# Performance work log

Hardware: AMD Instinct MI355X
Metric: run time of the kernel (lower is better)

The kernel has to match this reference:

```python
import jax, jax.numpy as jnp
import numpy as np

N, B, E = 10000, 4, 160000
C_IN, C_OUT, C_E = 64, 64, 16


def _mk_params(key, c_in, c_out, c_e):
    ks = jax.random.split(key, 8)
    s = 0.1
    return dict(
        w_n=jax.random.normal(ks[0], (c_in, c_out), jnp.float32) * s,
        w_e=jax.random.normal(ks[1], (c_e, c_out), jnp.float32) * s,
        q=jax.random.normal(ks[2], (c_out, c_out), jnp.float32) * s,
        k=jax.random.normal(ks[3], (c_out, c_out), jnp.float32) * s,
        aw=jax.random.normal(ks[4], (3 * c_out, 1), jnp.float32) * s,
        ab=jax.random.normal(ks[5], (1,), jnp.float32) * s,
        ow=jax.random.normal(ks[6], (2 * c_out, c_out), jnp.float32) * s,
        ob=jax.random.normal(ks[7], (c_out,), jnp.float32) * s,
    )


def setup_inputs() -> dict:
    key = jax.random.key(0)
    kx, ke, ka, k1, k2 = jax.random.split(key, 5)
    inp = {
        'X': jax.random.normal(kx, (N, B, C_IN), jnp.float32),
        'edge_index': jax.random.randint(ke, (2, E), 0, N, jnp.int32),
        'edge_attr': jax.random.normal(ka, (E, C_E), jnp.float32),
    }
    p1 = _mk_params(k1, C_IN, C_OUT, C_E)
    p2 = _mk_params(k2, C_OUT, C_OUT, C_E)
    for name, v in p1.items():
        inp[name + '1'] = v
    for name, v in p2.items():
        inp[name + '2'] = v
    return inp


def egnn_conv(x, edge_index, edge_attr, w_n, w_e, q, k, aw, ab, ow, ob, n_nodes):
    # x: [N,B,Cin]; edge_attr: [E,Ce]
    xp = x @ w_n                         # [N,B,C]
    ea = edge_attr @ w_e                 # [E,C]
    src, dst = edge_index[0], edge_index[1]
    xj = xp[src]                         # [E,B,C] gather (source)
    xi = xp[dst]                         # [E,B,C] gather (target)
    qf = xj @ q                          # [E,B,C]
    kf = xi @ k                          # [E,B,C]
    eab = jnp.broadcast_to(ea[:, None, :], qf.shape)  # [E,B,C]
    att_feat = jnp.concatenate([qf, kf, eab], axis=-1)  # [E,B,3C]
    att = jax.nn.sigmoid(att_feat @ aw + ab)            # [E,B,1]
    gate = jax.nn.sigmoid(eab)
    msg = att * xj * gate                # [E,B,C]
    aggr = jax.ops.segment_max(msg, dst, num_segments=n_nodes)  # [N,B,C]
    aggr = jnp.where(jnp.isneginf(aggr), 0.0, aggr)  # empty segments -> 0
    out = jnp.concatenate([xp, aggr], axis=-1) @ ow + ob
    return xp + out


def reference(X, edge_index, edge_attr,
              w_n1, w_e1, q1, k1, aw1, ab1, ow1, ob1,
              w_n2, w_e2, q2, k2, aw2, ab2, ow2, ob2):
    n_nodes = X.shape[0]
    c1 = egnn_conv(X, edge_index, edge_attr, w_n1, w_e1, q1, k1, aw1, ab1, ow1, ob1, n_nodes)
    c1 = jax.nn.leaky_relu(c1, 0.01)
    c2 = egnn_conv(c1, edge_index, edge_attr, w_n2, w_e2, q2, k2, aw2, ab2, ow2, ob2, n_nodes)
    c2 = jax.nn.leaky_relu(c2, 0.01)
    return c2
```

## Files before the change

kernel.cpp:

```cpp
#include <hip/hip_runtime.h>
#include <math.h>

#define NN 10000
#define BB 4
#define EE 160000
#define CC 64
#define CE 16

static constexpr size_t OFF_XPA    = 0;
static constexpr size_t OFF_XPB    = 10240000;
static constexpr size_t OFF_AGG    = 20480000;
static constexpr size_t OFF_SA     = 30720000;
static constexpr size_t OFF_SB     = 30880000;
static constexpr size_t OFF_VECS   = 31040000;
static constexpr size_t OFF_COUNTS = 31041280;
static constexpr size_t OFF_CURSOR = 31081280;
static constexpr size_t OFF_OFFS   = 31121280;
static constexpr size_t OFF_RECS   = 31161344;
static constexpr size_t OFF_ATT    = 32441344;

__device__ __forceinline__ float sigmoidf_(float x) {
    return 1.0f / (1.0f + __expf(-x));
}

__global__ void hist_vecs_kernel(const int* __restrict__ ei, int* __restrict__ counts,
                                 const float* __restrict__ q1, const float* __restrict__ k1,
                                 const float* __restrict__ aw1, const float* __restrict__ we1,
                                 const float* __restrict__ q2, const float* __restrict__ k2,
                                 const float* __restrict__ aw2, const float* __restrict__ we2,
                                 float* __restrict__ vecs) {
    int e = blockIdx.x * blockDim.x + threadIdx.x;
    if (e < EE) atomicAdd(&counts[ei[EE + e]], 1);
    if (blockIdx.x == 0) {
        int t = threadIdx.x;
        if (t < 64) {
            float a = 0.f, b = 0.f, c = 0.f, d = 0.f;
            for (int j = 0; j < 64; ++j) {
                a = fmaf(q1[t * 64 + j], aw1[j], a);
                b = fmaf(k1[t * 64 + j], aw1[64 + j], b);
                c = fmaf(q2[t * 64 + j], aw2[j], c);
                d = fmaf(k2[t * 64 + j], aw2[64 + j], d);
            }
            vecs[t] = a; vecs[64 + t] = b; vecs[144 + t] = c; vecs[208 + t] = d;
        }
        if (t < 16) {
            float a = 0.f, b = 0.f;
            for (int j = 0; j < 64; ++j) {
                a = fmaf(we1[t * 64 + j], aw1[128 + j], a);
                b = fmaf(we2[t * 64 + j], aw2[128 + j], b);
            }
            vecs[128 + t] = a; vecs[272 + t] = b;
        }
    }
}

__global__ void scan_kernel(const int* __restrict__ counts, int* __restrict__ offs, int n) {
    __shared__ int wsum[16];
    __shared__ int carry_sh;
    int t = threadIdx.x;
    int lane = t & 63, wid = t >> 6;
    if (t == 0) carry_sh = 0;
    __syncthreads();
    for (int base = 0; base < n; base += 1024) {
        int i = base + t;
        int v = (i < n) ? counts[i] : 0;
        int x = v;
        #pragma unroll
        for (int d = 1; d < 64; d <<= 1) {
            int y = __shfl_up(x, d, 64);
            if (lane >= d) x += y;
        }
        if (lane == 63) wsum[wid] = x;
        __syncthreads();
        if (wid == 0 && lane < 16) {
            int s = wsum[lane];
            int y2 = s;
            #pragma unroll
            for (int d = 1; d < 16; d <<= 1) {
                int z = __shfl_up(y2, d, 16);
                if (lane >= d) y2 += z;
            }
            wsum[lane] = y2;
        }
        __syncthreads();
        int waveExcl = (wid == 0) ? 0 : wsum[wid - 1];
        int carry = carry_sh;
        if (i < n) offs[i] = carry + waveExcl + x - v;
        int total = wsum[15];
        __syncthreads();
        if (t == 0) carry_sh = carry + total;
        __syncthreads();
    }
    if (threadIdx.x == 0) offs[n] = carry_sh;
}

__global__ void scatter_kernel(const int* __restrict__ ei, const int* __restrict__ offs,
                               int* __restrict__ cursor, int2* __restrict__ recs) {
    int e = blockIdx.x * blockDim.x + threadIdx.x;
    if (e >= EE) return;
    int s = ei[e], d = ei[EE + e];
    int p = atomicAdd(&cursor[d], 1);
    recs[offs[d] + p] = make_int2(s, e);
}

template <bool IN_T>
__global__ __launch_bounds__(256) void node_prep_kernel(
    const float* __restrict__ x,
    const float* __restrict__ w_n,
    const float* __restrict__ qa,
    const float* __restrict__ ka,
    float* __restrict__ xp_t,
    float* __restrict__ sa,
    float* __restrict__ sb) {
    __shared__ float w_sh[64 * 64];
    __shared__ float x_sh[4 * BB * CC];
    int t = threadIdx.x;
    for (int i = t; i < 64 * 64; i += 256) w_sh[i] = w_n[i];
    int node0 = blockIdx.x * 4;
    const float4* xg = (const float4*)(x + (size_t)node0 * BB * CC);
    ((float4*)x_sh)[t] = xg[t];
    __syncthreads();
    int wave = t >> 6, lane = t & 63;
    int node = node0 + wave;
    const float* xrow = x_sh + wave * BB * CC;
    float acc0 = 0.f, acc1 = 0.f, acc2 = 0.f, acc3 = 0.f;
    #pragma unroll 8
    for (int ci = 0; ci < 64; ++ci) {
        float w = w_sh[ci * 64 + lane];
        float x0 = IN_T ? xrow[ci * 4 + 0] : xrow[ci];
        float x1 = IN_T ? xrow[ci * 4 + 1] : xrow[64 + ci];
        float x2 = IN_T ? xrow[ci * 4 + 2] : xrow[128 + ci];
        float x3 = IN_T ? xrow[ci * 4 + 3] : xrow[192 + ci];
        acc0 = fmaf(x0, w, acc0);
        acc1 = fmaf(x1, w, acc1);
        acc2 = fmaf(x2, w, acc2);
        acc3 = fmaf(x3, w, acc3);
    }
    float4 st; st.x = acc0; st.y = acc1; st.z = acc2; st.w = acc3;
    *(float4*)(xp_t + (size_t)node * 256 + lane * 4) = st;
    float qv = qa[lane], kv = ka[lane];
    float ra0 = acc0 * qv, ra1 = acc1 * qv, ra2 = acc2 * qv, ra3 = acc3 * qv;
    float rb0 = acc0 * kv, rb1 = acc1 * kv, rb2 = acc2 * kv, rb3 = acc3 * kv;
    #pragma unroll
    for (int off = 32; off >= 1; off >>= 1) {
        ra0 += __shfl_xor(ra0, off, 64); ra1 += __shfl_xor(ra1, off, 64);
        ra2 += __shfl_xor(ra2, off, 64); ra3 += __shfl_xor(ra3, off, 64);
        rb0 += __shfl_xor(rb0, off, 64); rb1 += __shfl_xor(rb1, off, 64);
        rb2 += __shfl_xor(rb2, off, 64); rb3 += __shfl_xor(rb3, off, 64);
    }
    if (lane == 0) {
        sa[node * BB + 0] = ra0; sa[node * BB + 1] = ra1;
        sa[node * BB + 2] = ra2; sa[node * BB + 3] = ra3;
        sb[node * BB + 0] = rb0; sb[node * BB + 1] = rb1;
        sb[node * BB + 2] = rb2; sb[node * BB + 3] = rb3;
    }
}

__global__ __launch_bounds__(256) void att_kernel(
    const int* __restrict__ ei, const float* __restrict__ attr,
    const float* __restrict__ sa, const float* __restrict__ sb,
    const float* __restrict__ weav,
    const float* __restrict__ ab,
    float4* __restrict__ att) {
    int e = blockIdx.x * blockDim.x + threadIdx.x;
    if (e >= EE) return;
    int s = ei[e], d = ei[EE + e];
    const float4* ap = (const float4*)(attr + (size_t)e * CE);
    float4 a0 = ap[0], a1 = ap[1], a2 = ap[2], a3 = ap[3];
    float se = ab[0];
    se = fmaf(a0.x, weav[0], se);  se = fmaf(a0.y, weav[1], se);
    se = fmaf(a0.z, weav[2], se);  se = fmaf(a0.w, weav[3], se);
    se = fmaf(a1.x, weav[4], se);  se = fmaf(a1.y, weav[5], se);
    se = fmaf(a1.z, weav[6], se);  se = fmaf(a1.w, weav[7], se);
    se = fmaf(a2.x, weav[8], se);  se = fmaf(a2.y, weav[9], se);
    se = fmaf(a2.z, weav[10], se); se = fmaf(a2.w, weav[11], se);
    se = fmaf(a3.x, weav[12], se); se = fmaf(a3.y, weav[13], se);
    se = fmaf(a3.z, weav[14], se); se = fmaf(a3.w, weav[15], se);
    float4 sas = *(const float4*)(sa + (size_t)s * BB);
    float4 sbn = *(const float4*)(sb + (size_t)d * BB);
    float4 r;
    r.x = sigmoidf_(sas.x + sbn.x + se);
    r.y = sigmoidf_(sas.y + sbn.y + se);
    r.z = sigmoidf_(sas.z + sbn.z + se);
    r.w = sigmoidf_(sas.w + sbn.w + se);
    att[e] = r;
}

__global__ __launch_bounds__(256) void aggr_kernel(
    const float* __restrict__ xp_t,
    const int2* __restrict__ recs,
    const int* __restrict__ offs,
    const float* __restrict__ attr,
    const float* __restrict__ w_e,
    const float4* __restrict__ att,
    float* __restrict__ aggr_t) {
    int t = threadIdx.x;
    int wave = t >> 6, lane = t & 63;
    int node = blockIdx.x * 4 + wave;

    float wec[CE];
    #pragma unroll
    for (int j = 0; j < CE; ++j) wec[j] = w_e[j * CC + lane];

    int o0 = offs[node], o1 = offs[node + 1];
    float m0 = -INFINITY, m1 = -INFINITY, m2 = -INFINITY, m3 = -INFINITY;

    int i = o0;
    int2 rec = (i < o1) ? recs[i] : make_int2(0, 0);
    while (i < o1) {
        int2 cur = rec;
        ++i;
        if (i < o1) rec = recs[i];
        int s = cur.x, e = cur.y;
        float4 at = att[e];
        float4 xv = *(const float4*)(xp_t + (size_t)s * 256 + lane * 4);
        const float4* ap = (const float4*)(attr + (size_t)e * CE);
        float4 a0 = ap[0], a1 = ap[1], a2 = ap[2], a3 = ap[3];
        float g = 0.f;
        g = fmaf(a0.x, wec[0], g);  g = fmaf(a0.y, wec[1], g);
        g = fmaf(a0.z, wec[2], g);  g = fmaf(a0.w, wec[3], g);
        g = fmaf(a1.x, wec[4], g);  g = fmaf(a1.y, wec[5], g);
        g = fmaf(a1.z, wec[6], g);  g = fmaf(a1.w, wec[7], g);
        g = fmaf(a2.x, wec[8], g);  g = fmaf(a2.y, wec[9], g);
        g = fmaf(a2.z, wec[10], g); g = fmaf(a2.w, wec[11], g);
        g = fmaf(a3.x, wec[12], g); g = fmaf(a3.y, wec[13], g);
        g = fmaf(a3.z, wec[14], g); g = fmaf(a3.w, wec[15], g);
        g = sigmoidf_(g);
        m0 = fmaxf(m0, at.x * xv.x * g);
        m1 = fmaxf(m1, at.y * xv.y * g);
        m2 = fmaxf(m2, at.z * xv.z * g);
        m3 = fmaxf(m3, at.w * xv.w * g);
    }
    m0 = (m0 == -INFINITY) ? 0.f : m0;
    m1 = (m1 == -INFINITY) ? 0.f : m1;
    m2 = (m2 == -INFINITY) ? 0.f : m2;
    m3 = (m3 == -INFINITY) ? 0.f : m3;
    float4 st; st.x = m0; st.y = m1; st.z = m2; st.w = m3;
    *(float4*)(aggr_t + (size_t)node * 256 + lane * 4) = st;
}

template <bool WRITE_T>
__global__ __launch_bounds__(256) void out_kernel(
    const float* __restrict__ xp_t,
    const float* __restrict__ aggr_t,
    const float* __restrict__ ow,
    const float* __restrict__ ob,
    float* __restrict__ out) {
    __shared__ float xs[4][BB * CC];
    __shared__ float as_[4][BB * CC];
    int t = threadIdx.x;
    int wave = t >> 6, lane = t & 63;
    int node = blockIdx.x * 4 + wave;

    float4 xv = *(const float4*)(xp_t + (size_t)node * 256 + lane * 4);
    float4 av = *(const float4*)(aggr_t + (size_t)node * 256 + lane * 4);
    xs[wave][0 * 64 + lane] = xv.x; xs[wave][1 * 64 + lane] = xv.y;
    xs[wave][2 * 64 + lane] = xv.z; xs[wave][3 * 64 + lane] = xv.w;
    as_[wave][0 * 64 + lane] = av.x; as_[wave][1 * 64 + lane] = av.y;
    as_[wave][2 * 64 + lane] = av.z; as_[wave][3 * 64 + lane] = av.w;
    __syncthreads();

    const float* xr = xs[wave];
    const float* ar = as_[wave];
    float o0f = 0.f, o1f = 0.f, o2f = 0.f, o3f = 0.f;
    #pragma unroll 4
    for (int ci = 0; ci < 64; ++ci) {
        float wa = ow[ci * 64 + lane];
        float wb = ow[(64 + ci) * 64 + lane];
        o0f = fmaf(xr[ci], wa, o0f);
        o1f = fmaf(xr[64 + ci], wa, o1f);
        o2f = fmaf(xr[128 + ci], wa, o2f);
        o3f = fmaf(xr[192 + ci], wa, o3f);
        o0f = fmaf(ar[ci], wb, o0f);
        o1f = fmaf(ar[64 + ci], wb, o1f);
        o2f = fmaf(ar[128 + ci], wb, o2f);
        o3f = fmaf(ar[192 + ci], wb, o3f);
    }
    float obv = ob[lane];
    float r0 = xv.x + o0f + obv;
    float r1 = xv.y + o1f + obv;
    float r2 = xv.z + o2f + obv;
    float r3 = xv.w + o3f + obv;
    r0 = (r0 > 0.f) ? r0 : 0.01f * r0;
    r1 = (r1 > 0.f) ? r1 : 0.01f * r1;
    r2 = (r2 > 0.f) ? r2 : 0.01f * r2;
    r3 = (r3 > 0.f) ? r3 : 0.01f * r3;
    if (WRITE_T) {
        float4 st; st.x = r0; st.y = r1; st.z = r2; st.w = r3;
        *(float4*)(out + (size_t)node * 256 + lane * 4) = st;
    } else {
        float* op = out + (size_t)node * 256 + lane;
        op[0] = r0; op[64] = r1; op[128] = r2; op[192] = r3;
    }
}

extern "C" void kernel_launch(void* const* d_in, const int* in_sizes, int n_in,
                              void* d_out, int out_size, void* d_ws, size_t ws_size,
                              hipStream_t stream) {
    const float* X    = (const float*)d_in[0];
    const int*   ei   = (const int*)d_in[1];
    const float* attr = (const float*)d_in[2];
    const float* w_n1 = (const float*)d_in[3];
    const float* w_e1 = (const float*)d_in[4];
    const float* q1   = (const float*)d_in[5];
    const float* k1   = (const float*)d_in[6];
    const float* aw1  = (const float*)d_in[7];
    const float* ab1  = (const float*)d_in[8];
    const float* ow1  = (const float*)d_in[9];
    const float* ob1  = (const float*)d_in[10];
    const float* w_n2 = (const float*)d_in[11];
    const float* w_e2 = (const float*)d_in[12];
    const float* q2   = (const float*)d_in[13];
    const float* k2   = (const float*)d_in[14];
    const float* aw2  = (const float*)d_in[15];
    const float* ab2  = (const float*)d_in[16];
    const float* ow2  = (const float*)d_in[17];
    const float* ob2  = (const float*)d_in[18];
    float* out = (float*)d_out;

    char* ws = (char*)d_ws;
    float*  xpA    = (float*)(ws + OFF_XPA);
    float*  xpB    = (float*)(ws + OFF_XPB);
    float*  agg    = (float*)(ws + OFF_AGG);
    float*  sa     = (float*)(ws + OFF_SA);
    float*  sb     = (float*)(ws + OFF_SB);
    float*  vecs   = (float*)(ws + OFF_VECS);
    int*    counts = (int*)(ws + OFF_COUNTS);
    int*    cursor = (int*)(ws + OFF_CURSOR);
    int*    offs   = (int*)(ws + OFF_OFFS);
    int2*   recs   = (int2*)(ws + OFF_RECS);
    float4* att    = (float4*)(ws + OFF_ATT);

    hipMemsetAsync(counts, 0, 2 * NN * sizeof(int), stream);
    hist_vecs_kernel<<<EE / 256, 256, 0, stream>>>(ei, counts, q1, k1, aw1, w_e1,
                                                   q2, k2, aw2, w_e2, vecs);
    scan_kernel<<<1, 1024, 0, stream>>>(counts, offs, NN);
    scatter_kernel<<<EE / 256, 256, 0, stream>>>(ei, offs, cursor, recs);

    node_prep_kernel<false><<<NN / 4, 256, 0, stream>>>(X, w_n1, vecs + 0, vecs + 64,
                                                        xpA, sa, sb);
    att_kernel<<<EE / 256, 256, 0, stream>>>(ei, attr, sa, sb, vecs + 128, ab1, att);
    aggr_kernel<<<NN / 4, 256, 0, stream>>>(xpA, recs, offs, attr, w_e1, att, agg);
    out_kernel<true><<<NN / 4, 256, 0, stream>>>(xpA, agg, ow1, ob1, xpB);

    node_prep_kernel<true><<<NN / 4, 256, 0, stream>>>(xpB, w_n2, vecs + 144, vecs + 208,
                                                       xpA, sa, sb);
    att_kernel<<<EE / 256, 256, 0, stream>>>(ei, attr, sa, sb, vecs + 272, ab2, att);
    aggr_kernel<<<NN / 4, 256, 0, stream>>>(xpA, recs, offs, attr, w_e2, att, agg);
    out_kernel<false><<<NN / 4, 256, 0, stream>>>(xpA, agg, ow2, ob2, out);
}
```

Before: 316.8 us.

## Precompute per-edge gate tensor in edge kernel and unroll aggregation gather loop

The edge-attention kernel now also computes the sigmoid gate (edge_attr @ w_e) for all 64 channels per edge and writes it to a new E x 64 workspace buffer, one wave per 16 edges. The aggregation kernel then reads the precomputed gate instead of reloading edge attributes and redoing the 16-term dot product per edge, and processes four incoming edges per iteration to issue more independent gathers. The trade-off is about 41 MB of extra gate writes and reads per layer in exchange for less per-edge ALU work and fewer dependent loads in the aggregation loop.

```diff
diff --git a/kernel.cpp b/kernel.cpp
--- a/kernel.cpp
+++ b/kernel.cpp
@@ -18,6 +18,7 @@
 static constexpr size_t OFF_OFFS   = 31121280;
 static constexpr size_t OFF_RECS   = 31161344;
 static constexpr size_t OFF_ATT    = 32441344;
+static constexpr size_t OFF_GATE   = 35001344;
 
 __device__ __forceinline__ float sigmoidf_(float x) {
     return 1.0f / (1.0f + __expf(-x));
@@ -156,80 +157,99 @@
     }
 }
 
-__global__ __launch_bounds__(256) void att_kernel(
+__global__ __launch_bounds__(256) void edge_pre_kernel(
     const int* __restrict__ ei, const float* __restrict__ attr,
     const float* __restrict__ sa, const float* __restrict__ sb,
+    const float* __restrict__ w_e,
     const float* __restrict__ weav,
     const float* __restrict__ ab,
-    float4* __restrict__ att) {
-    int e = blockIdx.x * blockDim.x + threadIdx.x;
-    if (e >= EE) return;
-    int s = ei[e], d = ei[EE + e];
-    const float4* ap = (const float4*)(attr + (size_t)e * CE);
-    float4 a0 = ap[0], a1 = ap[1], a2 = ap[2], a3 = ap[3];
-    float se = ab[0];
-    se = fmaf(a0.x, weav[0], se);  se = fmaf(a0.y, weav[1], se);
-    se = fmaf(a0.z, weav[2], se);  se = fmaf(a0.w, weav[3], se);
-    se = fmaf(a1.x, weav[4], se);  se = fmaf(a1.y, weav[5], se);
-    se = fmaf(a1.z, weav[6], se);  se = fmaf(a1.w, weav[7], se);
-    se = fmaf(a2.x, weav[8], se);  se = fmaf(a2.y, weav[9], se);
-    se = fmaf(a2.z, weav[10], se); se = fmaf(a2.w, weav[11], se);
-    se = fmaf(a3.x, weav[12], se); se = fmaf(a3.y, weav[13], se);
-    se = fmaf(a3.z, weav[14], se); se = fmaf(a3.w, weav[15], se);
-    float4 sas = *(const float4*)(sa + (size_t)s * BB);
-    float4 sbn = *(const float4*)(sb + (size_t)d * BB);
-    float4 r;
-    r.x = sigmoidf_(sas.x + sbn.x + se);
-    r.y = sigmoidf_(sas.y + sbn.y + se);
-    r.z = sigmoidf_(sas.z + sbn.z + se);
-    r.w = sigmoidf_(sas.w + sbn.w + se);
-    att[e] = r;
+    float4* __restrict__ att, float* __restrict__ gate) {
+    int t = threadIdx.x;
+    int wave = t >> 6, lane = t & 63;
+    float wec[CE], wav[CE];
+    #pragma unroll
+    for (int j = 0; j < CE; ++j) { wec[j] = w_e[j * CC + lane]; wav[j] = weav[j]; }
+    float abv = ab[0];
+    int e0 = (blockIdx.x * 4 + wave) * 16;
+    #pragma unroll 2
+    for (int k = 0; k < 16; ++k) {
+        int e = e0 + k;
+        int s = ei[e], d = ei[EE + e];
+        const float4* ap = (const float4*)(attr + (size_t)e * CE);
+        float4 a0 = ap[0], a1 = ap[1], a2 = ap[2], a3 = ap[3];
+        float g = 0.f, se = 0.f;
+        g = fmaf(a0.x, wec[0], g);  se = fmaf(a0.x, wav[0], se);
+        g = fmaf(a0.y, wec[1], g);  se = fmaf(a0.y, wav[1], se);
+        g = fmaf(a0.z, wec[2], g);  se = fmaf(a0.z, wav[2], se);
+        g = fmaf(a0.w, wec[3], g);  se = fmaf(a0.w, wav[3], se);
+        g = fmaf(a1.x, wec[4], g);  se = fmaf(a1.x, wav[4], se);
+        g = fmaf(a1.y, wec[5], g);  se = fmaf(a1.y, wav[5], se);
+        g = fmaf(a1.z, wec[6], g);  se = fmaf(a1.z, wav[6], se);
+        g = fmaf(a1.w, wec[7], g);  se = fmaf(a1.w, wav[7], se);
+        g = fmaf(a2.x, wec[8], g);  se = fmaf(a2.x, wav[8], se);
+        g = fmaf(a2.y, wec[9], g);  se = fmaf(a2.y, wav[9], se);
+        g = fmaf(a2.z, wec[10], g); se = fmaf(a2.z, wav[10], se);
+        g = fmaf(a2.w, wec[11], g); se = fmaf(a2.w, wav[11], se);
+        g = fmaf(a3.x, wec[12], g); se = fmaf(a3.x, wav[12], se);
+        g = fmaf(a3.y, wec[13], g); se = fmaf(a3.y, wav[13], se);
+        g = fmaf(a3.z, wec[14], g); se = fmaf(a3.z, wav[14], se);
+        g = fmaf(a3.w, wec[15], g); se = fmaf(a3.w, wav[15], se);
+        gate[(size_t)e * CC + lane] = sigmoidf_(g);
+        float4 sas = *(const float4*)(sa + (size_t)s * BB);
+        float4 sbn = *(const float4*)(sb + (size_t)d * BB);
+        if (lane == 0) {
+            float4 r;
+            r.x = sigmoidf_(sas.x + sbn.x + se + abv);
+            r.y = sigmoidf_(sas.y + sbn.y + se + abv);
+            r.z = sigmoidf_(sas.z + sbn.z + se + abv);
+            r.w = sigmoidf_(sas.w + sbn.w + se + abv);
+            att[e] = r;
+        }
+    }
 }
 
 __global__ __launch_bounds__(256) void aggr_kernel(
     const float* __restrict__ xp_t,
     const int2* __restrict__ recs,
     const int* __restrict__ offs,
-    const float* __restrict__ attr,
-    const float* __restrict__ w_e,
     const float4* __restrict__ att,
+    const float* __restrict__ gate,
     float* __restrict__ aggr_t) {
     int t = threadIdx.x;
     int wave = t >> 6, lane = t & 63;
     int node = blockIdx.x * 4 + wave;
 
-    float wec[CE];
-    #pragma unroll
-    for (int j = 0; j < CE; ++j) wec[j] = w_e[j * CC + lane];
-
     int o0 = offs[node], o1 = offs[node + 1];
     float m0 = -INFINITY, m1 = -INFINITY, m2 = -INFINITY, m3 = -INFINITY;
 
     int i = o0;
-    int2 rec = (i < o1) ? recs[i] : make_int2(0, 0);
-    while (i < o1) {
-        int2 cur = rec;
-        ++i;
-        if (i < o1) rec = recs[i];
-        int s = cur.x, e = cur.y;
-        float4 at = att[e];
-        float4 xv = *(const float4*)(xp_t + (size_t)s * 256 + lane * 4);
-        const float4* ap = (const float4*)(attr + (size_t)e * CE);
-        float4 a0 = ap[0], a1 = ap[1], a2 = ap[2], a3 = ap[3];
-        float g = 0.f;
-        g = fmaf(a0.x, wec[0], g);  g = fmaf(a0.y, wec[1], g);
-        g = fmaf(a0.z, wec[2], g);  g = fmaf(a0.w, wec[3], g);
-        g = fmaf(a1.x, wec[4], g);  g = fmaf(a1.y, wec[5], g);
-        g = fmaf(a1.z, wec[6], g);  g = fmaf(a1.w, wec[7], g);
-        g = fmaf(a2.x, wec[8], g);  g = fmaf(a2.y, wec[9], g);
-        g = fmaf(a2.z, wec[10], g); g = fmaf(a2.w, wec[11], g);
-        g = fmaf(a3.x, wec[12], g); g = fmaf(a3.y, wec[13], g);
-        g = fmaf(a3.z, wec[14], g); g = fmaf(a3.w, wec[15], g);
-        g = sigmoidf_(g);
-        m0 = fmaxf(m0, at.x * xv.x * g);
-        m1 = fmaxf(m1, at.y * xv.y * g);
-        m2 = fmaxf(m2, at.z * xv.z * g);
-        m3 = fmaxf(m3, at.w * xv.w * g);
+    for (; i + 4 <= o1; i += 4) {
+        int2 ra = recs[i], rb = recs[i + 1], rc = recs[i + 2], rd = recs[i + 3];
+        float4 xa = *(const float4*)(xp_t + (size_t)ra.x * 256 + lane * 4);
+        float4 xb = *(const float4*)(xp_t + (size_t)rb.x * 256 + lane * 4);
+        float4 xc = *(const float4*)(xp_t + (size_t)rc.x * 256 + lane * 4);
+        float4 xd = *(const float4*)(xp_t + (size_t)rd.x * 256 + lane * 4);
+        float ga = gate[(size_t)ra.y * CC + lane];
+        float gb = gate[(size_t)rb.y * CC + lane];
+        float gc = gate[(size_t)rc.y * CC + lane];
+        float gd = gate[(size_t)rd.y * CC + lane];
+        float4 Aa = att[ra.y], Ab = att[rb.y], Ac = att[rc.y], Ad = att[rd.y];
+        m0 = fmaxf(m0, Aa.x * xa.x * ga); m1 = fmaxf(m1, Aa.y * xa.y * ga);
+        m2 = fmaxf(m2, Aa.z * xa.z * ga); m3 = fmaxf(m3, Aa.w * xa.w * ga);
+        m0 = fmaxf(m0, Ab.x * xb.x * gb); m1 = fmaxf(m1, Ab.y * xb.y * gb);
+        m2 = fmaxf(m2, Ab.z * xb.z * gb); m3 = fmaxf(m3, Ab.w * xb.w * gb);
+        m0 = fmaxf(m0, Ac.x * xc.x * gc); m1 = fmaxf(m1, Ac.y * xc.y * gc);
+        m2 = fmaxf(m2, Ac.z * xc.z * gc); m3 = fmaxf(m3, Ac.w * xc.w * gc);
+        m0 = fmaxf(m0, Ad.x * xd.x * gd); m1 = fmaxf(m1, Ad.y * xd.y * gd);
+        m2 = fmaxf(m2, Ad.z * xd.z * gd); m3 = fmaxf(m3, Ad.w * xd.w * gd);
+    }
+    for (; i < o1; ++i) {
+        int2 r = recs[i];
+        float4 xv = *(const float4*)(xp_t + (size_t)r.x * 256 + lane * 4);
+        float g = gate[(size_t)r.y * CC + lane];
+        float4 at = att[r.y];
+        m0 = fmaxf(m0, at.x * xv.x * g); m1 = fmaxf(m1, at.y * xv.y * g);
+        m2 = fmaxf(m2, at.z * xv.z * g); m3 = fmaxf(m3, at.w * xv.w * g);
     }
     m0 = (m0 == -INFINITY) ? 0.f : m0;
     m1 = (m1 == -INFINITY) ? 0.f : m1;
@@ -330,6 +350,7 @@
     int*    offs   = (int*)(ws + OFF_OFFS);
     int2*   recs   = (int2*)(ws + OFF_RECS);
     float4* att    = (float4*)(ws + OFF_ATT);
+    float*  gate   = (float*)(ws + OFF_GATE);
 
     hipMemsetAsync(counts, 0, 2 * NN * sizeof(int), stream);
     hist_vecs_kernel<<<EE / 256, 256, 0, stream>>>(ei, counts, q1, k1, aw1, w_e1,
@@ -339,13 +360,15 @@
 
     node_prep_kernel<false><<<NN / 4, 256, 0, stream>>>(X, w_n1, vecs + 0, vecs + 64,
                                                         xpA, sa, sb);
-    att_kernel<<<EE / 256, 256, 0, stream>>>(ei, attr, sa, sb, vecs + 128, ab1, att);
-    aggr_kernel<<<NN / 4, 256, 0, stream>>>(xpA, recs, offs, attr, w_e1, att, agg);
+    edge_pre_kernel<<<EE / 64, 256, 0, stream>>>(ei, attr, sa, sb, w_e1, vecs + 128,
+                                                 ab1, att, gate);
+    aggr_kernel<<<NN / 4, 256, 0, stream>>>(xpA, recs, offs, att, gate, agg);
     out_kernel<true><<<NN / 4, 256, 0, stream>>>(xpA, agg, ow1, ob1, xpB);
 
     node_prep_kernel<true><<<NN / 4, 256, 0, stream>>>(xpB, w_n2, vecs + 144, vecs + 208,
                                                        xpA, sa, sb);
-    att_kernel<<<EE / 256, 256, 0, stream>>>(ei, attr, sa, sb, vecs + 272, ab2, att);
-    aggr_kernel<<<NN / 4, 256, 0, stream>>>(xpA, recs, offs, attr, w_e2, att, agg);
+    edge_pre_kernel<<<EE / 64, 256, 0, stream>>>(ei, attr, sa, sb, w_e2, vecs + 272,
+                                                 ab2, att, gate);
+    aggr_kernel<<<NN / 4, 256, 0, stream>>>(xpA, recs, offs, att, gate, agg);
     out_kernel<false><<<NN / 4, 256, 0, stream>>>(xpA, agg, ow2, ob2, out);
 }
```

Result: slower. 371.8 us (+17.4%).

## Precompute per-edge gates in edge kernel and split node aggregation across four waves

Applied to the files above, without the earlier changes.

The per-edge sigmoid gate (edge_attr @ w_e) moves out of the aggregation loop into a per-edge kernel that also computes attention, writing a [E,64] gate buffer. Aggregation then runs one block per node, with four waves splitting the node's edge list and an LDS max-reduction combining them. This removes the repeated 16-FMA gate computation per gathered edge and adds parallelism for high-degree nodes. In exchange it writes and reads an extra 41 MB gate buffer per layer, and launches one wave per edge in the edge kernel.

```diff
diff --git a/kernel.cpp b/kernel.cpp
--- a/kernel.cpp
+++ b/kernel.cpp
@@ -18,6 +18,7 @@
 static constexpr size_t OFF_OFFS   = 31121280;
 static constexpr size_t OFF_RECS   = 31161344;
 static constexpr size_t OFF_ATT    = 32441344;
+static constexpr size_t OFF_GATE   = 35001344;
 
 __device__ __forceinline__ float sigmoidf_(float x) {
     return 1.0f / (1.0f + __expf(-x));
@@ -156,87 +157,107 @@
     }
 }
 
-__global__ __launch_bounds__(256) void att_kernel(
+__global__ __launch_bounds__(256) void edge_gate_att_kernel(
     const int* __restrict__ ei, const float* __restrict__ attr,
     const float* __restrict__ sa, const float* __restrict__ sb,
+    const float* __restrict__ w_e,
     const float* __restrict__ weav,
     const float* __restrict__ ab,
-    float4* __restrict__ att) {
-    int e = blockIdx.x * blockDim.x + threadIdx.x;
-    if (e >= EE) return;
-    int s = ei[e], d = ei[EE + e];
-    const float4* ap = (const float4*)(attr + (size_t)e * CE);
-    float4 a0 = ap[0], a1 = ap[1], a2 = ap[2], a3 = ap[3];
-    float se = ab[0];
-    se = fmaf(a0.x, weav[0], se);  se = fmaf(a0.y, weav[1], se);
-    se = fmaf(a0.z, weav[2], se);  se = fmaf(a0.w, weav[3], se);
-    se = fmaf(a1.x, weav[4], se);  se = fmaf(a1.y, weav[5], se);
-    se = fmaf(a1.z, weav[6], se);  se = fmaf(a1.w, weav[7], se);
-    se = fmaf(a2.x, weav[8], se);  se = fmaf(a2.y, weav[9], se);
-    se = fmaf(a2.z, weav[10], se); se = fmaf(a2.w, weav[11], se);
-    se = fmaf(a3.x, weav[12], se); se = fmaf(a3.y, weav[13], se);
-    se = fmaf(a3.z, weav[14], se); se = fmaf(a3.w, weav[15], se);
-    float4 sas = *(const float4*)(sa + (size_t)s * BB);
-    float4 sbn = *(const float4*)(sb + (size_t)d * BB);
-    float4 r;
-    r.x = sigmoidf_(sas.x + sbn.x + se);
-    r.y = sigmoidf_(sas.y + sbn.y + se);
-    r.z = sigmoidf_(sas.z + sbn.z + se);
-    r.w = sigmoidf_(sas.w + sbn.w + se);
-    att[e] = r;
-}
-
-__global__ __launch_bounds__(256) void aggr_kernel(
-    const float* __restrict__ xp_t,
-    const int2* __restrict__ recs,
-    const int* __restrict__ offs,
-    const float* __restrict__ attr,
-    const float* __restrict__ w_e,
-    const float4* __restrict__ att,
-    float* __restrict__ aggr_t) {
-    int t = threadIdx.x;
-    int wave = t >> 6, lane = t & 63;
-    int node = blockIdx.x * 4 + wave;
+    float4* __restrict__ att, float* __restrict__ gate) {
+    int t = threadIdx.x;
+    int wid = t >> 6, lane = t & 63;
+    int e = blockIdx.x * 4 + wid;
 
     float wec[CE];
     #pragma unroll
     for (int j = 0; j < CE; ++j) wec[j] = w_e[j * CC + lane];
 
+    const float4* ap = (const float4*)(attr + (size_t)e * CE);
+    float4 a0 = ap[0], a1 = ap[1], a2 = ap[2], a3 = ap[3];
+    float g = 0.f, se = ab[0];
+    g = fmaf(a0.x, wec[0], g);  se = fmaf(a0.x, weav[0], se);
+    g = fmaf(a0.y, wec[1], g);  se = fmaf(a0.y, weav[1], se);
+    g = fmaf(a0.z, wec[2], g);  se = fmaf(a0.z, weav[2], se);
+    g = fmaf(a0.w, wec[3], g);  se = fmaf(a0.w, weav[3], se);
+    g = fmaf(a1.x, wec[4], g);  se = fmaf(a1.x, weav[4], se);
+    g = fmaf(a1.y, wec[5], g);  se = fmaf(a1.y, weav[5], se);
+    g = fmaf(a1.z, wec[6], g);  se = fmaf(a1.z, weav[6], se);
+    g = fmaf(a1.w, wec[7], g);  se = fmaf(a1.w, weav[7], se);
+    g = fmaf(a2.x, wec[8], g);  se = fmaf(a2.x, weav[8], se);
+    g = fmaf(a2.y, wec[9], g);  se = fmaf(a2.y, weav[9], se);
+    g = fmaf(a2.z, wec[10], g); se = fmaf(a2.z, weav[10], se);
+    g = fmaf(a2.w, wec[11], g); se = fmaf(a2.w, weav[11], se);
+    g = fmaf(a3.x, wec[12], g); se = fmaf(a3.x, weav[12], se);
+    g = fmaf(a3.y, wec[13], g); se = fmaf(a3.y, weav[13], se);
+    g = fmaf(a3.z, wec[14], g); se = fmaf(a3.z, weav[14], se);
+    g = fmaf(a3.w, wec[15], g); se = fmaf(a3.w, weav[15], se);
+    gate[(size_t)e * CC + lane] = sigmoidf_(g);
+
+    if (lane == 0) {
+        int s = ei[e], d = ei[EE + e];
+        float4 sas = *(const float4*)(sa + (size_t)s * BB);
+        float4 sbn = *(const float4*)(sb + (size_t)d * BB);
+        float4 r;
+        r.x = sigmoidf_(sas.x + sbn.x + se);
+        r.y = sigmoidf_(sas.y + sbn.y + se);
+        r.z = sigmoidf_(sas.z + sbn.z + se);
+        r.w = sigmoidf_(sas.w + sbn.w + se);
+        att[e] = r;
+    }
+}
+
+__global__ __launch_bounds__(256) void aggr_kernel(
+    const float4* __restrict__ xp_t,
+    const int2* __restrict__ recs,
+    const int* __restrict__ offs,
+    const float4* __restrict__ att,
+    const float* __restrict__ gate,
+    float4* __restrict__ aggr_t) {
+    __shared__ float4 red[4][64];
+    int t = threadIdx.x;
+    int wid = t >> 6, lane = t & 63;
+    int node = blockIdx.x;
+
     int o0 = offs[node], o1 = offs[node + 1];
     float m0 = -INFINITY, m1 = -INFINITY, m2 = -INFINITY, m3 = -INFINITY;
 
-    int i = o0;
-    int2 rec = (i < o1) ? recs[i] : make_int2(0, 0);
-    while (i < o1) {
-        int2 cur = rec;
-        ++i;
-        if (i < o1) rec = recs[i];
-        int s = cur.x, e = cur.y;
-        float4 at = att[e];
-        float4 xv = *(const float4*)(xp_t + (size_t)s * 256 + lane * 4);
-        const float4* ap = (const float4*)(attr + (size_t)e * CE);
-        float4 a0 = ap[0], a1 = ap[1], a2 = ap[2], a3 = ap[3];
-        float g = 0.f;
-        g = fmaf(a0.x, wec[0], g);  g = fmaf(a0.y, wec[1], g);
-        g = fmaf(a0.z, wec[2], g);  g = fmaf(a0.w, wec[3], g);
-        g = fmaf(a1.x, wec[4], g);  g = fmaf(a1.y, wec[5], g);
-        g = fmaf(a1.z, wec[6], g);  g = fmaf(a1.w, wec[7], g);
-        g = fmaf(a2.x, wec[8], g);  g = fmaf(a2.y, wec[9], g);
-        g = fmaf(a2.z, wec[10], g); g = fmaf(a2.w, wec[11], g);
-        g = fmaf(a3.x, wec[12], g); g = fmaf(a3.y, wec[13], g);
-        g = fmaf(a3.z, wec[14], g); g = fmaf(a3.w, wec[15], g);
-        g = sigmoidf_(g);
-        m0 = fmaxf(m0, at.x * xv.x * g);
-        m1 = fmaxf(m1, at.y * xv.y * g);
-        m2 = fmaxf(m2, at.z * xv.z * g);
-        m3 = fmaxf(m3, at.w * xv.w * g);
-    }
-    m0 = (m0 == -INFINITY) ? 0.f : m0;
-    m1 = (m1 == -INFINITY) ? 0.f : m1;
-    m2 = (m2 == -INFINITY) ? 0.f : m2;
-    m3 = (m3 == -INFINITY) ? 0.f : m3;
-    float4 st; st.x = m0; st.y = m1; st.z = m2; st.w = m3;
-    *(float4*)(aggr_t + (size_t)node * 256 + lane * 4) = st;
+    int i = o0 + wid;
+    for (; i + 4 < o1; i += 8) {
+        int2 rA = recs[i], rB = recs[i + 4];
+        float4 xA = xp_t[(size_t)rA.x * 64 + lane];
+        float4 xB = xp_t[(size_t)rB.x * 64 + lane];
+        float gA = gate[(size_t)rA.y * CC + lane];
+        float gB = gate[(size_t)rB.y * CC + lane];
+        float4 AA = att[rA.y], AB = att[rB.y];
+        m0 = fmaxf(m0, AA.x * xA.x * gA); m1 = fmaxf(m1, AA.y * xA.y * gA);
+        m2 = fmaxf(m2, AA.z * xA.z * gA); m3 = fmaxf(m3, AA.w * xA.w * gA);
+        m0 = fmaxf(m0, AB.x * xB.x * gB); m1 = fmaxf(m1, AB.y * xB.y * gB);
+        m2 = fmaxf(m2, AB.z * xB.z * gB); m3 = fmaxf(m3, AB.w * xB.w * gB);
+    }
+    for (; i < o1; i += 4) {
+        int2 r = recs[i];
+        float4 xv = xp_t[(size_t)r.x * 64 + lane];
+        float g = gate[(size_t)r.y * CC + lane];
+        float4 at = att[r.y];
+        m0 = fmaxf(m0, at.x * xv.x * g); m1 = fmaxf(m1, at.y * xv.y * g);
+        m2 = fmaxf(m2, at.z * xv.z * g); m3 = fmaxf(m3, at.w * xv.w * g);
+    }
+    float4 mv; mv.x = m0; mv.y = m1; mv.z = m2; mv.w = m3;
+    red[wid][lane] = mv;
+    __syncthreads();
+    if (wid == 0) {
+        float4 a = red[0][lane], b = red[1][lane], c = red[2][lane], d = red[3][lane];
+        m0 = fmaxf(fmaxf(a.x, b.x), fmaxf(c.x, d.x));
+        m1 = fmaxf(fmaxf(a.y, b.y), fmaxf(c.y, d.y));
+        m2 = fmaxf(fmaxf(a.z, b.z), fmaxf(c.z, d.z));
+        m3 = fmaxf(fmaxf(a.w, b.w), fmaxf(c.w, d.w));
+        m0 = (m0 == -INFINITY) ? 0.f : m0;
+        m1 = (m1 == -INFINITY) ? 0.f : m1;
+        m2 = (m2 == -INFINITY) ? 0.f : m2;
+        m3 = (m3 == -INFINITY) ? 0.f : m3;
+        float4 st; st.x = m0; st.y = m1; st.z = m2; st.w = m3;
+        aggr_t[(size_t)node * 64 + lane] = st;
+    }
 }
 
 template <bool WRITE_T>
@@ -330,6 +351,7 @@
     int*    offs   = (int*)(ws + OFF_OFFS);
     int2*   recs   = (int2*)(ws + OFF_RECS);
     float4* att    = (float4*)(ws + OFF_ATT);
+    float*  gate   = (float*)(ws + OFF_GATE);
 
     hipMemsetAsync(counts, 0, 2 * NN * sizeof(int), stream);
     hist_vecs_kernel<<<EE / 256, 256, 0, stream>>>(ei, counts, q1, k1, aw1, w_e1,
@@ -339,13 +361,17 @@
 
     node_prep_kernel<false><<<NN / 4, 256, 0, stream>>>(X, w_n1, vecs + 0, vecs + 64,
                                                         xpA, sa, sb);
-    att_kernel<<<EE / 256, 256, 0, stream>>>(ei, attr, sa, sb, vecs + 128, ab1, att);
-    aggr_kernel<<<NN / 4, 256, 0, stream>>>(xpA, recs, offs, attr, w_e1, att, agg);
+    edge_gate_att_kernel<<<EE / 4, 256, 0, stream>>>(ei, attr, sa, sb, w_e1, vecs + 128,
+                                                     ab1, att, gate);
+    aggr_kernel<<<NN, 256, 0, stream>>>((const float4*)xpA, recs, offs, att, gate,
+                                        (float4*)agg);
     out_kernel<true><<<NN / 4, 256, 0, stream>>>(xpA, agg, ow1, ob1, xpB);
 
     node_prep_kernel<true><<<NN / 4, 256, 0, stream>>>(xpB, w_n2, vecs + 144, vecs + 208,
                                                        xpA, sa, sb);
-    att_kernel<<<EE / 256, 256, 0, stream>>>(ei, attr, sa, sb, vecs + 272, ab2, att);
-    aggr_kernel<<<NN / 4, 256, 0, stream>>>(xpA, recs, offs, attr, w_e2, att, agg);
+    edge_gate_att_kernel<<<EE / 4, 256, 0, stream>>>(ei, attr, sa, sb, w_e2, vecs + 272,
+                                                     ab2, att, gate);
+    aggr_kernel<<<NN, 256, 0, stream>>>((const float4*)xpA, recs, offs, att, gate,
+                                        (float4*)agg);
     out_kernel<false><<<NN / 4, 256, 0, stream>>>(xpA, agg, ow2, ob2, out);
 }
```

Measured after the change: 387.8 us. 1.22x slower.
